# Kernel optimization log

Measured on AMD Instinct MI355X. Metric: run time of the kernel, lower is better.

The kernel has to match this reference:

```python
import jax, jax.numpy as jnp
import numpy as np

B, C, H, Wd = 16, 256, 64, 64
D_MODEL = 256


def setup_inputs() -> dict:
    key = jax.random.key(0)
    kx, kw = jax.random.split(key)
    x = jax.random.normal(kx, (B, C, H, Wd), dtype=jnp.float32)
    # 1x1 conv weight [out_c=1+2*d_model, in_c], scaled like kaiming-ish init
    W = jax.random.normal(kw, (1 + 2 * D_MODEL, C), dtype=jnp.float32) / np.sqrt(C)
    return {"x": x, "W": W}


def reference(x, W):
    b, c, h, w = x.shape
    d = (W.shape[0] - 1) // 2
    n = h * w
    xf = x.reshape(b, c, n)                      # [b, c, N]
    qkv = jnp.einsum('oc,bcn->bon', W, xf)       # 1x1 conv == channel GEMM
    q = qkv[:, :1]                               # [b, 1, N]
    k = qkv[:, 1:1 + d]                          # [b, d, N]
    v = qkv[:, 1 + d:]                           # [b, d, N]
    scores = jax.nn.softmax(q, axis=-1)          # softmax over tokens
    ctx = jnp.sum(k * scores, axis=-1, keepdims=True)  # [b, d, 1]
    out = jax.nn.relu(v) * ctx                   # gated ReLU(v)
    return out.reshape(b, d, h, w)
```

## Files before the change

### kernel.cpp

```cpp
#include <hip/hip_runtime.h>
#include <cstdint>
#include <cstddef>

#define NB 16
#define NC 256
#define NN 4096
#define ND 256

typedef unsigned short u16;
typedef unsigned int u32;

typedef __attribute__((ext_vector_type(8))) short short8;
typedef __attribute__((ext_vector_type(4))) float f32x4;

__device__ __forceinline__ u16 f2bf(float f) {
  union { float f; u32 u; } v; v.f = f;
  u32 r = v.u + 0x7FFFu + ((v.u >> 16) & 1u);
  return (u16)(r >> 16);
}
__device__ __forceinline__ float bf2f(u16 h) {
  union { u32 u; float f; } v; v.u = ((u32)h) << 16; return v.f;
}

__global__ __launch_bounds__(256) void k_fuse1(const float* __restrict__ x,
                                               const float* __restrict__ W,
                                               u16* __restrict__ xbT,
                                               u16* __restrict__ wvb,
                                               float* __restrict__ pm,
                                               float* __restrict__ pl,
                                               float* __restrict__ pacc) {
  __shared__ float qred[32 * 65];
  __shared__ float qred2[4 * 65];
  const int t = threadIdx.x;
  const int b = blockIdx.y, n0 = blockIdx.x * 64;
  const int tx = t & 7, ty = t >> 3;
  const int c0 = ty * 8, nl = tx * 8;
  const float* xb = x + (size_t)b * NC * NN + n0;

  const float4 w0 = *(const float4*)(W + c0);
  const float4 w1 = *(const float4*)(W + c0 + 4);
  const float wq[8] = {w0.x, w0.y, w0.z, w0.w, w1.x, w1.y, w1.z, w1.w};

  short8 pk[8];
  float qp[8] = {0.f, 0.f, 0.f, 0.f, 0.f, 0.f, 0.f, 0.f};

#pragma unroll
  for (int r = 0; r < 8; ++r) {
    const float* xr = xb + (size_t)(c0 + r) * NN + nl;
    const float4 va = *(const float4*)(xr);
    const float4 vb = *(const float4*)(xr + 4);
    qp[0] += wq[r] * va.x; qp[1] += wq[r] * va.y;
    qp[2] += wq[r] * va.z; qp[3] += wq[r] * va.w;
    qp[4] += wq[r] * vb.x; qp[5] += wq[r] * vb.y;
    qp[6] += wq[r] * vb.z; qp[7] += wq[r] * vb.w;
    pk[0][r] = (short)f2bf(va.x); pk[1][r] = (short)f2bf(va.y);
    pk[2][r] = (short)f2bf(va.z); pk[3][r] = (short)f2bf(va.w);
    pk[4][r] = (short)f2bf(vb.x); pk[5][r] = (short)f2bf(vb.y);
    pk[6][r] = (short)f2bf(vb.z); pk[7][r] = (short)f2bf(vb.w);
  }

  u16* ob = xbT + (size_t)(b * NN + n0 + nl) * NC + c0;
#pragma unroll
  for (int j = 0; j < 8; ++j)
    *(short8*)(ob + (size_t)j * NC) = pk[j];

#pragma unroll
  for (int j = 0; j < 8; ++j) qred[ty * 65 + nl + j] = qp[j];
  __syncthreads();
  {
    const int n = t & 63, g = t >> 6;
    float s = 0.f;
#pragma unroll
    for (int k = 0; k < 8; ++k) s += qred[(g * 8 + k) * 65 + n];
    qred2[g * 65 + n] = s;
  }
  __syncthreads();

  float q[8];
#pragma unroll
  for (int j = 0; j < 8; ++j)
    q[j] = qred2[0 * 65 + nl + j] + qred2[1 * 65 + nl + j] +
           qred2[2 * 65 + nl + j] + qred2[3 * 65 + nl + j];

  float m = q[0];
#pragma unroll
  for (int j = 1; j < 8; ++j) m = fmaxf(m, q[j]);
#pragma unroll
  for (int off = 1; off < 8; off <<= 1) m = fmaxf(m, __shfl_xor(m, off));

  float p[8]; float l = 0.f;
#pragma unroll
  for (int j = 0; j < 8; ++j) { p[j] = __expf(q[j] - m); l += p[j]; }
#pragma unroll
  for (int off = 1; off < 8; off <<= 1) l += __shfl_xor(l, off);

  float sc[8];
#pragma unroll
  for (int r = 0; r < 8; ++r) {
    float s = 0.f;
#pragma unroll
    for (int j = 0; j < 8; ++j) s += bf2f((u16)pk[j][r]) * p[j];
    sc[r] = s;
  }
#pragma unroll
  for (int off = 1; off < 8; off <<= 1) {
#pragma unroll
    for (int r = 0; r < 8; ++r) sc[r] += __shfl_xor(sc[r], off);
  }
  if (tx == 0) {
    float* pp = pacc + ((size_t)b * 64 + blockIdx.x) * NC + c0;
#pragma unroll
    for (int r = 0; r < 8; ++r) pp[r] = sc[r];
  }
  if (t == 0) {
    pm[b * 64 + blockIdx.x] = m;
    pl[b * 64 + blockIdx.x] = l;
  }

  if (b == 0 && blockIdx.x < 8) {
    const float* wv = W + (size_t)(1 + ND) * NC;
    const int base = blockIdx.x * 8192;
#pragma unroll
    for (int i = 0; i < 8; ++i) {
      const int idx = base + i * 1024 + t * 4;
      const float4 v = *(const float4*)(wv + idx);
      ushort4 o = {f2bf(v.x), f2bf(v.y), f2bf(v.z), f2bf(v.w)};
      *(ushort4*)(wvb + idx) = o;
    }
  }
}

__global__ __launch_bounds__(256) void k_combine(const float* __restrict__ W,
                                                 const float* __restrict__ pm,
                                                 const float* __restrict__ pl,
                                                 const float* __restrict__ pacc,
                                                 float* __restrict__ ctx) {
  __shared__ float sm[64], sl[64], sw[64];
  __shared__ __align__(16) float sx[NC];
  const int b = blockIdx.x, t = threadIdx.x;
  if (t < 64) { sm[t] = pm[b * 64 + t]; sl[t] = pl[b * 64 + t]; }
  __syncthreads();
  float M = -3.4e38f;
#pragma unroll 16
  for (int i = 0; i < 64; ++i) M = fmaxf(M, sm[i]);
  if (t < 64) sw[t] = __expf(sm[t] - M);
  __syncthreads();
  float L = 0.f;
#pragma unroll 16
  for (int i = 0; i < 64; ++i) L += sw[i] * sl[i];
  float xsc = 0.f;
#pragma unroll 8
  for (int i = 0; i < 64; ++i) xsc += sw[i] * pacc[((size_t)b * 64 + i) * NC + t];
  sx[t] = xsc / L;
  __syncthreads();
  const float* wk = W + (size_t)(1 + t) * NC;
  float a = 0.f;
#pragma unroll 4
  for (int c4 = 0; c4 < 64; ++c4) {
    const float4 w4 = *(const float4*)(wk + c4 * 4);
    const float4 s4 = *(const float4*)&sx[c4 * 4];
    a += w4.x * s4.x + w4.y * s4.y + w4.z * s4.z + w4.w * s4.w;
  }
  ctx[b * NC + t] = a;
}

#define BM 256
#define BN 128
#define BK 64

__global__ __launch_bounds__(512) void k_gemm(const u16* __restrict__ xbT,
                                              const u16* __restrict__ wvb,
                                              const float* __restrict__ ctx,
                                              float* __restrict__ out) {
  __shared__ __align__(16) u16 As[BM * BK];
  __shared__ __align__(16) u16 Bs[BN * BK];
  const int t = threadIdx.x;
  const int b = blockIdx.y;
  const int n0 = blockIdx.x * BN;
  const int lane = t & 63, w = t >> 6;
  const int wd = (w >> 1) * 64, wn = (w & 1) * 64;
  const int quad = lane >> 4, l15 = lane & 15;

  f32x4 acc[4][4];
#pragma unroll
  for (int mi = 0; mi < 4; ++mi)
#pragma unroll
    for (int ni = 0; ni < 4; ++ni)
      acc[mi][ni] = (f32x4){0.f, 0.f, 0.f, 0.f};

  const int rstg = t >> 3;
  const int l8 = ((t & 7) ^ (rstg & 7)) * 8;
  const u16* gA = wvb + (size_t)rstg * NC + l8;
  const u16* gB = xbT + (size_t)(b * NN + n0 + rstg) * NC + l8;
  const int ldst = 8 * t;

  const int pq0 = ((0 * 4 + quad) ^ (l15 & 7)) * 8;
  const int pq1 = ((1 * 4 + quad) ^ (l15 & 7)) * 8;

  for (int kk = 0; kk < NC; kk += BK) {
    __syncthreads();
#pragma unroll
    for (int i = 0; i < 4; ++i)
      __builtin_amdgcn_global_load_lds(
          (const __attribute__((address_space(1))) u32*)(gA + kk + (size_t)(64 * i) * NC),
          (__attribute__((address_space(3))) u32*)(As + 4096 * i + ldst), 16, 0, 0);
#pragma unroll
    for (int i = 0; i < 2; ++i)
      __builtin_amdgcn_global_load_lds(
          (const __attribute__((address_space(1))) u32*)(gB + kk + (size_t)(64 * i) * NC),
          (__attribute__((address_space(3))) u32*)(Bs + 4096 * i + ldst), 16, 0, 0);
    __syncthreads();

#pragma unroll
    for (int kq = 0; kq < 2; ++kq) {
      const int pq = kq ? pq1 : pq0;
      short8 af[4], bfr[4];
#pragma unroll
      for (int mi = 0; mi < 4; ++mi)
        af[mi] = *(const short8*)&As[(wd + mi * 16 + l15) * BK + pq];
#pragma unroll
      for (int ni = 0; ni < 4; ++ni)
        bfr[ni] = *(const short8*)&Bs[(wn + ni * 16 + l15) * BK + pq];
#pragma unroll
      for (int mi = 0; mi < 4; ++mi)
#pragma unroll
        for (int ni = 0; ni < 4; ++ni)
          acc[mi][ni] = __builtin_amdgcn_mfma_f32_16x16x32_bf16(af[mi], bfr[ni],
                                                                acc[mi][ni], 0, 0, 0);
    }
  }

#pragma unroll
  for (int mi = 0; mi < 4; ++mi) {
#pragma unroll
    for (int r = 0; r < 4; ++r) {
      const int d = wd + mi * 16 + quad * 4 + r;
      const float cx = ctx[b * NC + d];
      float* op = out + (size_t)(b * NC + d) * NN + n0 + wn + l15;
#pragma unroll
      for (int ni = 0; ni < 4; ++ni) {
        float v = acc[mi][ni][r];
        op[ni * 16] = fmaxf(v, 0.f) * cx;
      }
    }
  }
}

extern "C" void kernel_launch(void* const* d_in, const int* in_sizes, int n_in,
                              void* d_out, int out_size, void* d_ws, size_t ws_size,
                              hipStream_t stream) {
  const float* x = (const float*)d_in[0];
  const float* W = (const float*)d_in[1];
  float* out = (float*)d_out;

  char* ws = (char*)d_ws;
  u16* xbT    = (u16*)ws;
  float* pacc = (float*)(ws + 33554432);
  float* pm   = (float*)(ws + 34603008);
  float* pl   = (float*)(ws + 34607104);
  float* ctx  = (float*)(ws + 34611200);
  u16* wvb    = (u16*)(ws + 34627584);

  k_fuse1<<<dim3(64, 16), 256, 0, stream>>>(x, W, xbT, wvb, pm, pl, pacc);
  k_combine<<<16, 256, 0, stream>>>(W, pm, pl, pacc, ctx);
  k_gemm<<<dim3(32, 16), 512, 0, stream>>>(xbT, wvb, ctx, out);
}
```

Before: 150.5 us.

## Fuse three kernels into one cooperative kernel keeping bf16 x tile in LDS

Replaces the three-kernel pipeline with a single cooperative kernel of 256 blocks. Each block converts its 256-token slab of x to bf16 into a swizzled 128KB LDS tile, computes the local softmax partials, and does a grid-wide sync for the cross-block combine. It then runs the value GEMM straight from LDS, with W_v read from global memory. This removes the 32MB global round-trip of the transposed bf16 x and two launches, at the cost of a grid barrier, low occupancy from the large LDS footprint, and a cooperative-launch residency requirement.

```diff
diff --git a/kernel.cpp b/kernel.cpp
--- a/kernel.cpp
+++ b/kernel.cpp
@@ -1,4 +1,5 @@
 #include <hip/hip_runtime.h>
+#include <hip/hip_cooperative_groups.h>
 #include <cstdint>
 #include <cstddef>
 
@@ -22,212 +23,183 @@
   union { u32 u; float f; } v; v.u = ((u32)h) << 16; return v.f;
 }
 
-__global__ __launch_bounds__(256) void k_fuse1(const float* __restrict__ x,
-                                               const float* __restrict__ W,
-                                               u16* __restrict__ xbT,
-                                               u16* __restrict__ wvb,
-                                               float* __restrict__ pm,
-                                               float* __restrict__ pl,
-                                               float* __restrict__ pacc) {
-  __shared__ float qred[32 * 65];
-  __shared__ float qred2[4 * 65];
+__global__ __launch_bounds__(512) void k_mono(const float* __restrict__ x,
+                                              const float* __restrict__ W,
+                                              float* __restrict__ out,
+                                              float* __restrict__ pacc,
+                                              float* __restrict__ pm,
+                                              float* __restrict__ pl,
+                                              u16* __restrict__ wvb) {
+  namespace cg = cooperative_groups;
+  cg::grid_group grid = cg::this_grid();
+
+  __shared__ __align__(16) u16 xt[256 * 256];
+  __shared__ float qred[16 * 257];
+  __shared__ float pv[256];
+  __shared__ float pp2[2 * 257];
+  __shared__ float am[16], al[16];
+  __shared__ float sx[256];
+  __shared__ float sctx[256];
+  __shared__ float wredm[8], wredl[8];
+
   const int t = threadIdx.x;
-  const int b = blockIdx.y, n0 = blockIdx.x * 64;
-  const int tx = t & 7, ty = t >> 3;
-  const int c0 = ty * 8, nl = tx * 8;
-  const float* xb = x + (size_t)b * NC * NN + n0;
-
-  const float4 w0 = *(const float4*)(W + c0);
-  const float4 w1 = *(const float4*)(W + c0 + 4);
-  const float wq[8] = {w0.x, w0.y, w0.z, w0.w, w1.x, w1.y, w1.z, w1.w};
-
-  short8 pk[8];
+  const int g = blockIdx.x;
+  const int b = g >> 4;
+  const int n0 = (g & 15) << 8;
+
+  const int tx = t & 31;
+  const int ty = t >> 5;
+  const int nl = tx * 8;
+
   float qp[8] = {0.f, 0.f, 0.f, 0.f, 0.f, 0.f, 0.f, 0.f};
 
-#pragma unroll
-  for (int r = 0; r < 8; ++r) {
-    const float* xr = xb + (size_t)(c0 + r) * NN + nl;
-    const float4 va = *(const float4*)(xr);
-    const float4 vb = *(const float4*)(xr + 4);
-    qp[0] += wq[r] * va.x; qp[1] += wq[r] * va.y;
-    qp[2] += wq[r] * va.z; qp[3] += wq[r] * va.w;
-    qp[4] += wq[r] * vb.x; qp[5] += wq[r] * vb.y;
-    qp[6] += wq[r] * vb.z; qp[7] += wq[r] * vb.w;
-    pk[0][r] = (short)f2bf(va.x); pk[1][r] = (short)f2bf(va.y);
-    pk[2][r] = (short)f2bf(va.z); pk[3][r] = (short)f2bf(va.w);
-    pk[4][r] = (short)f2bf(vb.x); pk[5][r] = (short)f2bf(vb.y);
-    pk[6][r] = (short)f2bf(vb.z); pk[7][r] = (short)f2bf(vb.w);
-  }
-
-  u16* ob = xbT + (size_t)(b * NN + n0 + nl) * NC + c0;
-#pragma unroll
-  for (int j = 0; j < 8; ++j)
-    *(short8*)(ob + (size_t)j * NC) = pk[j];
-
-#pragma unroll
-  for (int j = 0; j < 8; ++j) qred[ty * 65 + nl + j] = qp[j];
-  __syncthreads();
+  for (int i = 0; i < 2; ++i) {
+    const int c0 = ty * 8 + i * 128;
+    const float4 w0 = *(const float4*)(W + c0);
+    const float4 w1 = *(const float4*)(W + c0 + 4);
+    const float wq[8] = {w0.x, w0.y, w0.z, w0.w, w1.x, w1.y, w1.z, w1.w};
+    short8 pk[8];
+#pragma unroll
+    for (int r = 0; r < 8; ++r) {
+      const float* xr = x + (size_t)(b * NC + c0 + r) * NN + n0 + nl;
+      const float4 va = *(const float4*)(xr);
+      const float4 vb = *(const float4*)(xr + 4);
+      qp[0] += wq[r] * va.x; qp[1] += wq[r] * va.y;
+      qp[2] += wq[r] * va.z; qp[3] += wq[r] * va.w;
+      qp[4] += wq[r] * vb.x; qp[5] += wq[r] * vb.y;
+      qp[6] += wq[r] * vb.z; qp[7] += wq[r] * vb.w;
+      pk[0][r] = (short)f2bf(va.x); pk[1][r] = (short)f2bf(va.y);
+      pk[2][r] = (short)f2bf(va.z); pk[3][r] = (short)f2bf(va.w);
+      pk[4][r] = (short)f2bf(vb.x); pk[5][r] = (short)f2bf(vb.y);
+      pk[6][r] = (short)f2bf(vb.z); pk[7][r] = (short)f2bf(vb.w);
+    }
+    const int chunk = ty + i * 16;
+#pragma unroll
+    for (int jn = 0; jn < 8; ++jn) {
+      const int n = nl + jn;
+      const int phys = chunk ^ (n & 7) ^ ((n >> 3) & 7);
+      *(short8*)&xt[n * 256 + phys * 8] = pk[jn];
+    }
+  }
+
+#pragma unroll
+  for (int jn = 0; jn < 8; ++jn) qred[ty * 257 + nl + jn] = qp[jn];
+  __syncthreads();
+
+  float q = 0.f;
+  if (t < 256) {
+#pragma unroll
+    for (int k = 0; k < 16; ++k) q += qred[k * 257 + t];
+  }
+  float wm = (t < 256) ? q : -3.4e38f;
+#pragma unroll
+  for (int off = 1; off < 64; off <<= 1) wm = fmaxf(wm, __shfl_xor(wm, off));
+  const int wvn = t >> 6;
+  if ((t & 63) == 0 && wvn < 4) wredm[wvn] = wm;
+  __syncthreads();
+  const float M = fmaxf(fmaxf(wredm[0], wredm[1]), fmaxf(wredm[2], wredm[3]));
+  float p = 0.f;
+  if (t < 256) { p = __expf(q - M); pv[t] = p; }
+  float wl = (t < 256) ? p : 0.f;
+#pragma unroll
+  for (int off = 1; off < 64; off <<= 1) wl += __shfl_xor(wl, off);
+  if ((t & 63) == 0 && wvn < 4) wredl[wvn] = wl;
+  __syncthreads();
+  const float Lc = wredl[0] + wredl[1] + wredl[2] + wredl[3];
+
   {
-    const int n = t & 63, g = t >> 6;
-    float s = 0.f;
-#pragma unroll
-    for (int k = 0; k < 8; ++k) s += qred[(g * 8 + k) * 65 + n];
-    qred2[g * 65 + n] = s;
-  }
-  __syncthreads();
-
-  float q[8];
-#pragma unroll
-  for (int j = 0; j < 8; ++j)
-    q[j] = qred2[0 * 65 + nl + j] + qred2[1 * 65 + nl + j] +
-           qred2[2 * 65 + nl + j] + qred2[3 * 65 + nl + j];
-
-  float m = q[0];
-#pragma unroll
-  for (int j = 1; j < 8; ++j) m = fmaxf(m, q[j]);
-#pragma unroll
-  for (int off = 1; off < 8; off <<= 1) m = fmaxf(m, __shfl_xor(m, off));
-
-  float p[8]; float l = 0.f;
-#pragma unroll
-  for (int j = 0; j < 8; ++j) { p[j] = __expf(q[j] - m); l += p[j]; }
-#pragma unroll
-  for (int off = 1; off < 8; off <<= 1) l += __shfl_xor(l, off);
-
-  float sc[8];
-#pragma unroll
-  for (int r = 0; r < 8; ++r) {
-    float s = 0.f;
-#pragma unroll
-    for (int j = 0; j < 8; ++j) s += bf2f((u16)pk[j][r]) * p[j];
-    sc[r] = s;
-  }
-#pragma unroll
-  for (int off = 1; off < 8; off <<= 1) {
-#pragma unroll
-    for (int r = 0; r < 8; ++r) sc[r] += __shfl_xor(sc[r], off);
-  }
-  if (tx == 0) {
-    float* pp = pacc + ((size_t)b * 64 + blockIdx.x) * NC + c0;
-#pragma unroll
-    for (int r = 0; r < 8; ++r) pp[r] = sc[r];
-  }
-  if (t == 0) {
-    pm[b * 64 + blockIdx.x] = m;
-    pl[b * 64 + blockIdx.x] = l;
-  }
-
-  if (b == 0 && blockIdx.x < 8) {
-    const float* wv = W + (size_t)(1 + ND) * NC;
-    const int base = blockIdx.x * 8192;
-#pragma unroll
-    for (int i = 0; i < 8; ++i) {
-      const int idx = base + i * 1024 + t * 4;
-      const float4 v = *(const float4*)(wv + idx);
-      ushort4 o = {f2bf(v.x), f2bf(v.y), f2bf(v.z), f2bf(v.w)};
-      *(ushort4*)(wvb + idx) = o;
-    }
-  }
-}
-
-__global__ __launch_bounds__(256) void k_combine(const float* __restrict__ W,
-                                                 const float* __restrict__ pm,
-                                                 const float* __restrict__ pl,
-                                                 const float* __restrict__ pacc,
-                                                 float* __restrict__ ctx) {
-  __shared__ float sm[64], sl[64], sw[64];
-  __shared__ __align__(16) float sx[NC];
-  const int b = blockIdx.x, t = threadIdx.x;
-  if (t < 64) { sm[t] = pm[b * 64 + t]; sl[t] = pl[b * 64 + t]; }
-  __syncthreads();
-  float M = -3.4e38f;
-#pragma unroll 16
-  for (int i = 0; i < 64; ++i) M = fmaxf(M, sm[i]);
-  if (t < 64) sw[t] = __expf(sm[t] - M);
-  __syncthreads();
-  float L = 0.f;
-#pragma unroll 16
-  for (int i = 0; i < 64; ++i) L += sw[i] * sl[i];
-  float xsc = 0.f;
+    const int cc = t & 255, hh = t >> 8;
+    const int cchunk = cc >> 3, clo = cc & 7;
+    float aps = 0.f;
 #pragma unroll 8
-  for (int i = 0; i < 64; ++i) xsc += sw[i] * pacc[((size_t)b * 64 + i) * NC + t];
-  sx[t] = xsc / L;
-  __syncthreads();
-  const float* wk = W + (size_t)(1 + t) * NC;
-  float a = 0.f;
+    for (int nn2 = 0; nn2 < 128; ++nn2) {
+      const int n = hh * 128 + nn2;
+      const int phys = cchunk ^ (n & 7) ^ ((n >> 3) & 7);
+      aps += bf2f(xt[n * 256 + phys * 8 + clo]) * pv[n];
+    }
+    pp2[hh * 257 + cc] = aps;
+  }
+  __syncthreads();
+  if (t < 256) pacc[(size_t)g * 256 + t] = pp2[t] + pp2[257 + t];
+  if (t == 0) { pm[g] = M; pl[g] = Lc; }
+
+  if (g < 16) {
+    const float* wsrc = W + (size_t)(1 + ND) * NC + (size_t)g * 16 * NC;
+    const int idx = t * 8;
+    const float4 a0 = *(const float4*)(wsrc + idx);
+    const float4 a1 = *(const float4*)(wsrc + idx + 4);
+    short8 o;
+    o[0] = (short)f2bf(a0.x); o[1] = (short)f2bf(a0.y);
+    o[2] = (short)f2bf(a0.z); o[3] = (short)f2bf(a0.w);
+    o[4] = (short)f2bf(a1.x); o[5] = (short)f2bf(a1.y);
+    o[6] = (short)f2bf(a1.z); o[7] = (short)f2bf(a1.w);
+    *(short8*)(wvb + (size_t)g * 4096 + idx) = o;
+  }
+
+  __threadfence();
+  grid.sync();
+  __threadfence();
+
+  if (t < 16) { am[t] = pm[b * 16 + t]; al[t] = pl[b * 16 + t]; }
+  __syncthreads();
+  float M2 = -3.4e38f;
+#pragma unroll
+  for (int i = 0; i < 16; ++i) M2 = fmaxf(M2, am[i]);
+  if (t < 256) {
+    float xsv = 0.f, L2s = 0.f;
+#pragma unroll
+    for (int i = 0; i < 16; ++i) {
+      const float wgt = __expf(am[i] - M2);
+      L2s += wgt * al[i];
+      xsv += wgt * pacc[(size_t)(b * 16 + i) * 256 + t];
+    }
+    sx[t] = xsv / L2s;
+  }
+  __syncthreads();
+  if (t < 256) {
+    const float* wk = W + (size_t)(1 + t) * NC;
+    float a = 0.f;
 #pragma unroll 4
-  for (int c4 = 0; c4 < 64; ++c4) {
-    const float4 w4 = *(const float4*)(wk + c4 * 4);
-    const float4 s4 = *(const float4*)&sx[c4 * 4];
-    a += w4.x * s4.x + w4.y * s4.y + w4.z * s4.z + w4.w * s4.w;
-  }
-  ctx[b * NC + t] = a;
-}
-
-#define BM 256
-#define BN 128
-#define BK 64
-
-__global__ __launch_bounds__(512) void k_gemm(const u16* __restrict__ xbT,
-                                              const u16* __restrict__ wvb,
-                                              const float* __restrict__ ctx,
-                                              float* __restrict__ out) {
-  __shared__ __align__(16) u16 As[BM * BK];
-  __shared__ __align__(16) u16 Bs[BN * BK];
-  const int t = threadIdx.x;
-  const int b = blockIdx.y;
-  const int n0 = blockIdx.x * BN;
+    for (int c4 = 0; c4 < 64; ++c4) {
+      const float4 w4 = *(const float4*)(wk + c4 * 4);
+      const float4 s4 = *(const float4*)&sx[c4 * 4];
+      a += w4.x * s4.x + w4.y * s4.y + w4.z * s4.z + w4.w * s4.w;
+    }
+    sctx[t] = a;
+  }
+  __syncthreads();
+
   const int lane = t & 63, w = t >> 6;
-  const int wd = (w >> 1) * 64, wn = (w & 1) * 64;
+  const int wd = (w >> 1) * 64, wn = (w & 1) * 128;
   const int quad = lane >> 4, l15 = lane & 15;
 
-  f32x4 acc[4][4];
+  f32x4 acc[4][8];
 #pragma unroll
   for (int mi = 0; mi < 4; ++mi)
 #pragma unroll
-    for (int ni = 0; ni < 4; ++ni)
+    for (int ni = 0; ni < 8; ++ni)
       acc[mi][ni] = (f32x4){0.f, 0.f, 0.f, 0.f};
 
-  const int rstg = t >> 3;
-  const int l8 = ((t & 7) ^ (rstg & 7)) * 8;
-  const u16* gA = wvb + (size_t)rstg * NC + l8;
-  const u16* gB = xbT + (size_t)(b * NN + n0 + rstg) * NC + l8;
-  const int ldst = 8 * t;
-
-  const int pq0 = ((0 * 4 + quad) ^ (l15 & 7)) * 8;
-  const int pq1 = ((1 * 4 + quad) ^ (l15 & 7)) * 8;
-
-  for (int kk = 0; kk < NC; kk += BK) {
-    __syncthreads();
-#pragma unroll
-    for (int i = 0; i < 4; ++i)
-      __builtin_amdgcn_global_load_lds(
-          (const __attribute__((address_space(1))) u32*)(gA + kk + (size_t)(64 * i) * NC),
-          (__attribute__((address_space(3))) u32*)(As + 4096 * i + ldst), 16, 0, 0);
-#pragma unroll
-    for (int i = 0; i < 2; ++i)
-      __builtin_amdgcn_global_load_lds(
-          (const __attribute__((address_space(1))) u32*)(gB + kk + (size_t)(64 * i) * NC),
-          (__attribute__((address_space(3))) u32*)(Bs + 4096 * i + ldst), 16, 0, 0);
-    __syncthreads();
-
-#pragma unroll
-    for (int kq = 0; kq < 2; ++kq) {
-      const int pq = kq ? pq1 : pq0;
-      short8 af[4], bfr[4];
-#pragma unroll
-      for (int mi = 0; mi < 4; ++mi)
-        af[mi] = *(const short8*)&As[(wd + mi * 16 + l15) * BK + pq];
-#pragma unroll
-      for (int ni = 0; ni < 4; ++ni)
-        bfr[ni] = *(const short8*)&Bs[(wn + ni * 16 + l15) * BK + pq];
-#pragma unroll
-      for (int mi = 0; mi < 4; ++mi)
-#pragma unroll
-        for (int ni = 0; ni < 4; ++ni)
-          acc[mi][ni] = __builtin_amdgcn_mfma_f32_16x16x32_bf16(af[mi], bfr[ni],
-                                                                acc[mi][ni], 0, 0, 0);
-    }
+#pragma unroll
+  for (int kq = 0; kq < 8; ++kq) {
+    short8 af[4];
+#pragma unroll
+    for (int mi = 0; mi < 4; ++mi)
+      af[mi] = *(const short8*)(wvb + (size_t)(wd + mi * 16 + l15) * NC +
+                                kq * 32 + quad * 8);
+    short8 bfr[8];
+#pragma unroll
+    for (int ni = 0; ni < 8; ++ni) {
+      const int n = wn + ni * 16 + l15;
+      const int phys = (kq * 4 + quad) ^ (n & 7) ^ ((n >> 3) & 7);
+      bfr[ni] = *(const short8*)&xt[n * 256 + phys * 8];
+    }
+#pragma unroll
+    for (int mi = 0; mi < 4; ++mi)
+#pragma unroll
+      for (int ni = 0; ni < 8; ++ni)
+        acc[mi][ni] = __builtin_amdgcn_mfma_f32_16x16x32_bf16(af[mi], bfr[ni],
+                                                              acc[mi][ni], 0, 0, 0);
   }
 
 #pragma unroll
@@ -235,13 +207,11 @@
 #pragma unroll
     for (int r = 0; r < 4; ++r) {
       const int d = wd + mi * 16 + quad * 4 + r;
-      const float cx = ctx[b * NC + d];
+      const float cx = sctx[d];
       float* op = out + (size_t)(b * NC + d) * NN + n0 + wn + l15;
 #pragma unroll
-      for (int ni = 0; ni < 4; ++ni) {
-        float v = acc[mi][ni][r];
-        op[ni * 16] = fmaxf(v, 0.f) * cx;
-      }
+      for (int ni = 0; ni < 8; ++ni)
+        op[ni * 16] = fmaxf(acc[mi][ni][r], 0.f) * cx;
     }
   }
 }
@@ -254,14 +224,13 @@
   float* out = (float*)d_out;
 
   char* ws = (char*)d_ws;
-  u16* xbT    = (u16*)ws;
-  float* pacc = (float*)(ws + 33554432);
-  float* pm   = (float*)(ws + 34603008);
-  float* pl   = (float*)(ws + 34607104);
-  float* ctx  = (float*)(ws + 34611200);
-  u16* wvb    = (u16*)(ws + 34627584);
-
-  k_fuse1<<<dim3(64, 16), 256, 0, stream>>>(x, W, xbT, wvb, pm, pl, pacc);
-  k_combine<<<16, 256, 0, stream>>>(W, pm, pl, pacc, ctx);
-  k_gemm<<<dim3(32, 16), 512, 0, stream>>>(xbT, wvb, ctx, out);
-}
+  float* pacc = (float*)ws;
+  float* pm   = (float*)(ws + 262144);
+  float* pl   = (float*)(ws + 263168);
+  u16* wvb    = (u16*)(ws + 264192);
+
+  void* args[] = {(void*)&x, (void*)&W, (void*)&out,
+                  (void*)&pacc, (void*)&pm, (void*)&pl, (void*)&wvb};
+  hipLaunchCooperativeKernel((void*)k_mono, dim3(256), dim3(512), args, 0,
+                             stream);
+}
```

Result: slower. 232.7 us (+54.6%).

## Fuse context combine into GEMM and vectorize epilogue stores via operand swap

Applied to the files above, without the earlier changes.

Removes the separate combine kernel by having every GEMM block recompute the softmax-weighted context vector in shared memory, overlapped with the first tile prefetch. Swaps MFMA operand order so each lane owns four consecutive tokens, enabling float4 nontemporal output stores. Trades one kernel launch and global ctx round trip for redundant per-block reduction work and extra reads of W and partial sums.

```diff
diff --git a/kernel.cpp b/kernel.cpp
--- a/kernel.cpp
+++ b/kernel.cpp
@@ -130,50 +130,23 @@
   }
 }
 
-__global__ __launch_bounds__(256) void k_combine(const float* __restrict__ W,
-                                                 const float* __restrict__ pm,
-                                                 const float* __restrict__ pl,
-                                                 const float* __restrict__ pacc,
-                                                 float* __restrict__ ctx) {
-  __shared__ float sm[64], sl[64], sw[64];
-  __shared__ __align__(16) float sx[NC];
-  const int b = blockIdx.x, t = threadIdx.x;
-  if (t < 64) { sm[t] = pm[b * 64 + t]; sl[t] = pl[b * 64 + t]; }
-  __syncthreads();
-  float M = -3.4e38f;
-#pragma unroll 16
-  for (int i = 0; i < 64; ++i) M = fmaxf(M, sm[i]);
-  if (t < 64) sw[t] = __expf(sm[t] - M);
-  __syncthreads();
-  float L = 0.f;
-#pragma unroll 16
-  for (int i = 0; i < 64; ++i) L += sw[i] * sl[i];
-  float xsc = 0.f;
-#pragma unroll 8
-  for (int i = 0; i < 64; ++i) xsc += sw[i] * pacc[((size_t)b * 64 + i) * NC + t];
-  sx[t] = xsc / L;
-  __syncthreads();
-  const float* wk = W + (size_t)(1 + t) * NC;
-  float a = 0.f;
-#pragma unroll 4
-  for (int c4 = 0; c4 < 64; ++c4) {
-    const float4 w4 = *(const float4*)(wk + c4 * 4);
-    const float4 s4 = *(const float4*)&sx[c4 * 4];
-    a += w4.x * s4.x + w4.y * s4.y + w4.z * s4.z + w4.w * s4.w;
-  }
-  ctx[b * NC + t] = a;
-}
-
 #define BM 256
 #define BN 128
 #define BK 64
 
 __global__ __launch_bounds__(512) void k_gemm(const u16* __restrict__ xbT,
                                               const u16* __restrict__ wvb,
-                                              const float* __restrict__ ctx,
+                                              const float* __restrict__ W,
+                                              const float* __restrict__ pm,
+                                              const float* __restrict__ pl,
+                                              const float* __restrict__ pacc,
                                               float* __restrict__ out) {
   __shared__ __align__(16) u16 As[BM * BK];
   __shared__ __align__(16) u16 Bs[BN * BK];
+  __shared__ float am[64], al[64];
+  __shared__ __align__(16) float sx[NC];
+  __shared__ float sctx[NC];
+
   const int t = threadIdx.x;
   const int b = blockIdx.y;
   const int n0 = blockIdx.x * BN;
@@ -181,67 +154,110 @@
   const int wd = (w >> 1) * 64, wn = (w & 1) * 64;
   const int quad = lane >> 4, l15 = lane & 15;
 
-  f32x4 acc[4][4];
-#pragma unroll
-  for (int mi = 0; mi < 4; ++mi)
-#pragma unroll
-    for (int ni = 0; ni < 4; ++ni)
-      acc[mi][ni] = (f32x4){0.f, 0.f, 0.f, 0.f};
-
   const int rstg = t >> 3;
   const int l8 = ((t & 7) ^ (rstg & 7)) * 8;
   const u16* gA = wvb + (size_t)rstg * NC + l8;
   const u16* gB = xbT + (size_t)(b * NN + n0 + rstg) * NC + l8;
   const int ldst = 8 * t;
 
+#pragma unroll
+  for (int i = 0; i < 4; ++i)
+    __builtin_amdgcn_global_load_lds(
+        (const __attribute__((address_space(1))) u32*)(gA + (size_t)(64 * i) * NC),
+        (__attribute__((address_space(3))) u32*)(As + 4096 * i + ldst), 16, 0, 0);
+#pragma unroll
+  for (int i = 0; i < 2; ++i)
+    __builtin_amdgcn_global_load_lds(
+        (const __attribute__((address_space(1))) u32*)(gB + (size_t)(64 * i) * NC),
+        (__attribute__((address_space(3))) u32*)(Bs + 4096 * i + ldst), 16, 0, 0);
+
+  if (t < 64) { am[t] = pm[b * 64 + t]; al[t] = pl[b * 64 + t]; }
+  __syncthreads();
+
+  float M2 = -3.4e38f;
+#pragma unroll
+  for (int i = 0; i < 64; ++i) M2 = fmaxf(M2, am[i]);
+  if (t < 256) {
+    float xsv = 0.f, L2s = 0.f;
+#pragma unroll 8
+    for (int i = 0; i < 64; ++i) {
+      const float wgt = __expf(am[i] - M2);
+      L2s += wgt * al[i];
+      xsv += wgt * pacc[(size_t)(b * 64 + i) * NC + t];
+    }
+    sx[t] = xsv / L2s;
+  }
+  __syncthreads();
+  if (t < 256) {
+    const float* wk = W + (size_t)(1 + t) * NC;
+    float a = 0.f;
+#pragma unroll 4
+    for (int c4 = 0; c4 < 64; ++c4) {
+      const float4 w4 = *(const float4*)(wk + c4 * 4);
+      const float4 s4 = *(const float4*)&sx[c4 * 4];
+      a += w4.x * s4.x + w4.y * s4.y + w4.z * s4.z + w4.w * s4.w;
+    }
+    sctx[t] = a;
+  }
+
+  f32x4 acc[4][4];
+#pragma unroll
+  for (int ni = 0; ni < 4; ++ni)
+#pragma unroll
+    for (int mi = 0; mi < 4; ++mi)
+      acc[ni][mi] = (f32x4){0.f, 0.f, 0.f, 0.f};
+
   const int pq0 = ((0 * 4 + quad) ^ (l15 & 7)) * 8;
   const int pq1 = ((1 * 4 + quad) ^ (l15 & 7)) * 8;
 
   for (int kk = 0; kk < NC; kk += BK) {
-    __syncthreads();
-#pragma unroll
-    for (int i = 0; i < 4; ++i)
-      __builtin_amdgcn_global_load_lds(
-          (const __attribute__((address_space(1))) u32*)(gA + kk + (size_t)(64 * i) * NC),
-          (__attribute__((address_space(3))) u32*)(As + 4096 * i + ldst), 16, 0, 0);
-#pragma unroll
-    for (int i = 0; i < 2; ++i)
-      __builtin_amdgcn_global_load_lds(
-          (const __attribute__((address_space(1))) u32*)(gB + kk + (size_t)(64 * i) * NC),
-          (__attribute__((address_space(3))) u32*)(Bs + 4096 * i + ldst), 16, 0, 0);
-    __syncthreads();
+    if (kk) {
+      __syncthreads();
+#pragma unroll
+      for (int i = 0; i < 4; ++i)
+        __builtin_amdgcn_global_load_lds(
+            (const __attribute__((address_space(1))) u32*)(gA + kk + (size_t)(64 * i) * NC),
+            (__attribute__((address_space(3))) u32*)(As + 4096 * i + ldst), 16, 0, 0);
+#pragma unroll
+      for (int i = 0; i < 2; ++i)
+        __builtin_amdgcn_global_load_lds(
+            (const __attribute__((address_space(1))) u32*)(gB + kk + (size_t)(64 * i) * NC),
+            (__attribute__((address_space(3))) u32*)(Bs + 4096 * i + ldst), 16, 0, 0);
+      __syncthreads();
+    }
 
 #pragma unroll
     for (int kq = 0; kq < 2; ++kq) {
       const int pq = kq ? pq1 : pq0;
-      short8 af[4], bfr[4];
+      short8 xf[4], wf[4];
+#pragma unroll
+      for (int ni = 0; ni < 4; ++ni)
+        xf[ni] = *(const short8*)&Bs[(wn + ni * 16 + l15) * BK + pq];
 #pragma unroll
       for (int mi = 0; mi < 4; ++mi)
-        af[mi] = *(const short8*)&As[(wd + mi * 16 + l15) * BK + pq];
+        wf[mi] = *(const short8*)&As[(wd + mi * 16 + l15) * BK + pq];
 #pragma unroll
       for (int ni = 0; ni < 4; ++ni)
-        bfr[ni] = *(const short8*)&Bs[(wn + ni * 16 + l15) * BK + pq];
-#pragma unroll
-      for (int mi = 0; mi < 4; ++mi)
-#pragma unroll
-        for (int ni = 0; ni < 4; ++ni)
-          acc[mi][ni] = __builtin_amdgcn_mfma_f32_16x16x32_bf16(af[mi], bfr[ni],
-                                                                acc[mi][ni], 0, 0, 0);
+#pragma unroll
+        for (int mi = 0; mi < 4; ++mi)
+          acc[ni][mi] = __builtin_amdgcn_mfma_f32_16x16x32_bf16(xf[ni], wf[mi],
+                                                                acc[ni][mi], 0, 0, 0);
     }
   }
 
 #pragma unroll
   for (int mi = 0; mi < 4; ++mi) {
-#pragma unroll
-    for (int r = 0; r < 4; ++r) {
-      const int d = wd + mi * 16 + quad * 4 + r;
-      const float cx = ctx[b * NC + d];
-      float* op = out + (size_t)(b * NC + d) * NN + n0 + wn + l15;
-#pragma unroll
-      for (int ni = 0; ni < 4; ++ni) {
-        float v = acc[mi][ni][r];
-        op[ni * 16] = fmaxf(v, 0.f) * cx;
-      }
+    const int d = wd + mi * 16 + l15;
+    const float cx = sctx[d];
+    float* op = out + (size_t)(b * NC + d) * NN + n0 + wn + quad * 4;
+#pragma unroll
+    for (int ni = 0; ni < 4; ++ni) {
+      f32x4 v = acc[ni][mi];
+      v[0] = fmaxf(v[0], 0.f) * cx;
+      v[1] = fmaxf(v[1], 0.f) * cx;
+      v[2] = fmaxf(v[2], 0.f) * cx;
+      v[3] = fmaxf(v[3], 0.f) * cx;
+      __builtin_nontemporal_store(v, (f32x4*)(op + ni * 16));
     }
   }
 }
@@ -258,10 +274,8 @@
   float* pacc = (float*)(ws + 33554432);
   float* pm   = (float*)(ws + 34603008);
   float* pl   = (float*)(ws + 34607104);
-  float* ctx  = (float*)(ws + 34611200);
-  u16* wvb    = (u16*)(ws + 34627584);
+  u16* wvb    = (u16*)(ws + 34611200);
 
   k_fuse1<<<dim3(64, 16), 256, 0, stream>>>(x, W, xbT, wvb, pm, pl, pacc);
-  k_combine<<<16, 256, 0, stream>>>(W, pm, pl, pacc, ctx);
-  k_gemm<<<dim3(32, 16), 512, 0, stream>>>(xbT, wvb, ctx, out);
-}
+  k_gemm<<<dim3(32, 16), 512, 0, stream>>>(xbT, wvb, W, pm, pl, pacc, out);
+}
```

New measurement: 154.0 us. 2.3% more time.
